# Performance work log

Hardware: AMD Instinct MI355X
Metric: run time of the kernel (lower is better)

Reference implementation:

```python
import jax, jax.numpy as jnp
import numpy as np


def adder2d(x, w, stride=1, padding=0):
    """AdderNet conv: out = -sum_{ci,kh,kw} |x_patch - w|, supports groups.
    x: [B,Cin,H,W], w: [Cout, Cin//G, K, K]. Loops only over K*K kernel taps."""
    B, Cin, H, W = x.shape
    Cout, Cin_g, K, _ = w.shape
    G = Cin // Cin_g
    Co_g = Cout // G
    xp = jnp.pad(x, ((0, 0), (0, 0), (padding, padding), (padding, padding)))
    Ho = (H + 2 * padding - K) // stride + 1
    Wo = (W + 2 * padding - K) // stride + 1
    wg = w.reshape(G, Co_g, Cin_g, K, K)
    out = jnp.zeros((B, Cout, Ho, Wo), x.dtype)
    for kh in range(K):
        for kw in range(K):
            xs = jax.lax.slice(
                xp, (0, 0, kh, kw),
                (B, Cin, kh + stride * (Ho - 1) + 1, kw + stride * (Wo - 1) + 1),
                (1, 1, stride, stride))  # [B,Cin,Ho,Wo]
            xs = xs.reshape(B, G, 1, Cin_g, Ho, Wo)
            wt = wg[:, :, :, kh, kw][None, :, :, :, None, None]  # [1,G,Co_g,Cin_g,1,1]
            out = out - jnp.abs(xs - wt).sum(3).reshape(B, Cout, Ho, Wo)
    return out


def bn(x, g, b, m, v, eps=1e-5):
    inv = g / jnp.sqrt(v + eps)
    return x * inv[None, :, None, None] + (b - m * inv)[None, :, None, None]


def setup_inputs() -> dict:
    key = jax.random.key(0)
    ks = jax.random.split(key, 18)
    d = {}
    d["x"] = jax.random.normal(ks[0], (8, 256, 28, 28), jnp.float32)
    d["w1"] = jax.random.normal(ks[1], (64, 256, 1, 1), jnp.float32) * 0.05
    d["w_peg"] = jax.random.normal(ks[2], (64, 1, 3, 3), jnp.float32) * 0.05
    d["w2"] = jax.random.normal(ks[3], (64, 64, 3, 3), jnp.float32) * 0.05
    d["w3"] = jax.random.normal(ks[4], (256, 64, 1, 1), jnp.float32) * 0.05
    for i, (c, tag) in enumerate([(64, "1"), (64, "2"), (256, "3")]):
        d["g" + tag] = jax.random.uniform(ks[5 + 4 * i], (c,), jnp.float32, 0.5, 1.5)
        d["b" + tag] = jax.random.normal(ks[6 + 4 * i], (c,), jnp.float32) * 0.1
        d["m" + tag] = jax.random.normal(ks[7 + 4 * i], (c,), jnp.float32) * 0.1
        d["v" + tag] = jax.random.uniform(ks[8 + 4 * i], (c,), jnp.float32, 0.5, 1.5)
    return d


def reference(x, w1, w_peg, w2, w3, g1, b1, m1, v1, g2, b2, m2, v2, g3, b3, m3, v3):
    residual = x  # downsample is Identity (stride=1, inplanes==outplanes)
    h = adder2d(x, w1)                       # 1x1 adder conv 256->64
    h = adder2d(h, w_peg, stride=1, padding=1)  # PEG: depthwise 3x3 adder conv
    h = jax.nn.relu(bn(h, g1, b1, m1, v1))
    h = adder2d(h, w2, padding=1)            # 3x3 adder conv 64->64
    h = jax.nn.relu(bn(h, g2, b2, m2, v2))
    h = adder2d(h, w3)                       # 1x1 adder conv 64->256
    h = bn(h, g3, b3, m3, v3)
    return jax.nn.relu(h + residual)
```

## Files before the change

### kernel.cpp

```cpp
#include <hip/hip_runtime.h>
#include <math.h>

#define PR 30
#define PC 32

__device__ __forceinline__ void tap3(const float4 a, const float2 b,
                                     const float w0, const float w1, const float w2,
                                     float4& acc) {
    acc.x += fabsf(a.x - w0) + fabsf(a.y - w1) + fabsf(a.z - w2);
    acc.y += fabsf(a.y - w0) + fabsf(a.z - w1) + fabsf(a.w - w2);
    acc.z += fabsf(a.z - w0) + fabsf(a.w - w1) + fabsf(b.x - w2);
    acc.w += fabsf(a.w - w0) + fabsf(b.x - w1) + fabsf(b.y - w2);
}

__global__ __launch_bounds__(448) void ka_fused(const float* __restrict__ x,
                                                const float* __restrict__ w1,
                                                const float* __restrict__ wpeg,
                                                const float* __restrict__ w2,
                                                const float* __restrict__ w3,
                                                const float* __restrict__ g1,
                                                const float* __restrict__ b1,
                                                const float* __restrict__ m1,
                                                const float* __restrict__ v1,
                                                float* __restrict__ h2p,
                                                float* __restrict__ w2t,
                                                float* __restrict__ w3t) {
    __shared__ __align__(16) float smem[3072];
    float* wsA = smem;
    float* h1t = smem + 1024;
    const int tid    = threadIdx.x;
    const int cobase = blockIdx.x * 4;
    const int yh     = blockIdx.y;
    const int n      = blockIdx.z;
    const int co     = tid / 112;
    const int rem    = tid % 112;
    const int row    = rem / 7;
    const int q      = rem % 7;

    {
        const int bid3 = blockIdx.x + 16 * (blockIdx.y + 2 * blockIdx.z);
        const int tg = bid3 * 448 + tid;
        if (tg < 36864) {
            int r = tg >> 6, c2 = tg & 63;
            w2t[tg] = w2[(size_t)c2 * 576 + r];
        } else if (tg < 53248) {
            int i = tg - 36864;
            int ci = i >> 8, c2 = i & 255;
            w3t[i] = w3[(size_t)c2 * 64 + ci];
        }
    }

    for (int idx = tid; idx < 1024; idx += 448) {
        int c2 = idx >> 8, ci = idx & 255;
        wsA[ci * 4 + c2] = w1[(size_t)(cobase + c2) * 256 + ci];
    }
    for (int idx = tid; idx < 512; idx += 448)
        ((float4*)h1t)[idx] = make_float4(0.f, 0.f, 0.f, 0.f);
    __syncthreads();

    const int gy = yh * 14 - 1 + row;
    if (gy >= 0 && gy < 28) {
        float4 acc = {0.f, 0.f, 0.f, 0.f};
        const float* xp = x + (size_t)n * 256 * 784 + gy * 28 + q * 4;
        #pragma unroll 8
        for (int ci = 0; ci < 256; ++ci) {
            float4 u = *(const float4*)(xp + (size_t)ci * 784);
            float w  = wsA[ci * 4 + co];
            acc.x += fabsf(u.x - w); acc.y += fabsf(u.y - w);
            acc.z += fabsf(u.z - w); acc.w += fabsf(u.w - w);
        }
        float* hd = h1t + co * 512 + row * 32 + 1 + q * 4;
        hd[0] = -acc.x; hd[1] = -acc.y; hd[2] = -acc.z; hd[3] = -acc.w;
    }
    __syncthreads();

    if (row < 14) {
        const int c  = cobase + co;
        const int oy = yh * 14 + row;
        const float* wc = wpeg + c * 9;
        const float* hb = h1t + co * 512 + row * 32 + q * 4;
        float4 acc = {0.f, 0.f, 0.f, 0.f};
        #pragma unroll
        for (int kh = 0; kh < 3; ++kh) {
            float4 a  = *(const float4*)(hb + kh * 32);
            float2 bv = *(const float2*)(hb + kh * 32 + 4);
            tap3(a, bv, wc[kh * 3 + 0], wc[kh * 3 + 1], wc[kh * 3 + 2], acc);
        }
        float inv = g1[c] * rsqrtf(v1[c] + 1e-5f);
        float bb  = b1[c] - m1[c] * inv;
        float* op = h2p + ((size_t)(n * 64 + c) * PR + oy + 1) * PC + 1 + q * 4;
        op[0] = fmaxf(-acc.x * inv + bb, 0.f);
        op[1] = fmaxf(-acc.y * inv + bb, 0.f);
        op[2] = fmaxf(-acc.z * inv + bb, 0.f);
        op[3] = fmaxf(-acc.w * inv + bb, 0.f);
    }
    for (int idx = tid; idx < 352; idx += 448) {
        if (idx < 224) {
            int rr = idx >> 4, k = idx & 15;
            int cc = k >> 2, kk = k & 3;
            int col = kk ? 28 + kk : 0;
            h2p[((size_t)(n * 64 + cobase + cc) * PR + yh * 14 + 1 + rr) * PC + col] = 0.f;
        } else {
            int j = idx - 224;
            int cc = j >> 5, col = j & 31;
            int prow = yh ? 29 : 0;
            h2p[((size_t)(n * 64 + cobase + cc) * PR + prow) * PC + col] = 0.f;
        }
    }
}

__device__ __forceinline__ void red4(float4& v, int mask) {
    v.x += __shfl_xor(v.x, mask, 64);
    v.y += __shfl_xor(v.y, mask, 64);
    v.z += __shfl_xor(v.z, mask, 64);
    v.w += __shfl_xor(v.w, mask, 64);
}

__global__ __launch_bounds__(512) void kb_fused(const float* __restrict__ h2p,
                                                const float* __restrict__ w2t,
                                                const float* __restrict__ w3t,
                                                const float* __restrict__ x,
                                                const float* __restrict__ g2,
                                                const float* __restrict__ b2,
                                                const float* __restrict__ m2,
                                                const float* __restrict__ v2,
                                                const float* __restrict__ g3,
                                                const float* __restrict__ b3,
                                                const float* __restrict__ m3,
                                                const float* __restrict__ v3,
                                                float* __restrict__ out) {
    __shared__ __align__(16) float h2t[6400];
    __shared__ __align__(16) float h3t[1280];
    const int tid  = threadIdx.x;
    const int half = blockIdx.x;
    const int Y    = blockIdx.y;
    const int n    = blockIdx.z;
    const int cic    = tid & 7;
    const int q      = (tid >> 3) & 3;
    const int colane = tid >> 5;
    const int pxb    = half * 12;

    for (int iq = tid; iq < 1536; iq += 512) {
        int ci = iq / 24, r2 = iq % 24;
        int r = r2 >> 3, c4 = r2 & 7;
        *(float4*)(h2t + ci * 100 + r * 32 + c4 * 4) =
            *(const float4*)(h2p + ((size_t)(n * 64 + ci) * PR + Y + r) * PC + c4 * 4);
    }
    __syncthreads();

    float4 acc0 = {0,0,0,0}, acc1 = acc0, acc2 = acc0, acc3 = acc0;
    #pragma unroll 2
    for (int ci8 = 0; ci8 < 8; ++ci8) {
        const int ci = ci8 * 8 + cic;
        const float* hb = h2t + ci * 100 + pxb + q * 4;
        const float* wr = w2t + (size_t)ci * 576 + colane * 4;
        #pragma unroll
        for (int kh = 0; kh < 3; ++kh) {
            float4 a  = *(const float4*)(hb + kh * 32);
            float2 bv = *(const float2*)(hb + kh * 32 + 4);
            float4 W0 = *(const float4*)(wr + (kh * 3 + 0) * 64);
            float4 W1 = *(const float4*)(wr + (kh * 3 + 1) * 64);
            float4 W2 = *(const float4*)(wr + (kh * 3 + 2) * 64);
            tap3(a, bv, W0.x, W1.x, W2.x, acc0);
            tap3(a, bv, W0.y, W1.y, W2.y, acc1);
            tap3(a, bv, W0.z, W1.z, W2.z, acc2);
            tap3(a, bv, W0.w, W1.w, W2.w, acc3);
        }
    }
    red4(acc0, 1); red4(acc0, 2); red4(acc0, 4);
    red4(acc1, 1); red4(acc1, 2); red4(acc1, 4);
    red4(acc2, 1); red4(acc2, 2); red4(acc2, 4);
    red4(acc3, 1); red4(acc3, 2); red4(acc3, 4);
    if (cic < 4) {
        float4 s = (cic == 0) ? acc0 : (cic == 1) ? acc1 : (cic == 2) ? acc2 : acc3;
        const int co = colane * 4 + cic;
        float inv = g2[co] * rsqrtf(v2[co] + 1e-5f);
        float bb  = b2[co] - m2[co] * inv;
        float4 o;
        o.x = fmaxf(-s.x * inv + bb, 0.f);
        o.y = fmaxf(-s.y * inv + bb, 0.f);
        o.z = fmaxf(-s.z * inv + bb, 0.f);
        o.w = fmaxf(-s.w * inv + bb, 0.f);
        *(float4*)(h3t + co * 20 + q * 4) = o;
    }
    __syncthreads();

    {
        const int bl  = tid >> 3;
        const int cih = (tid >> 2) & 1;
        const int bq  = tid & 3;
        float4 a0 = {0,0,0,0}, a1 = a0, a2 = a0, a3 = a0;
        const float* hb = h3t + cih * 32 * 20 + bq * 4;
        const float* wb = w3t + (size_t)(cih * 32) * 256 + bl * 4;
        #pragma unroll 8
        for (int ci_l = 0; ci_l < 32; ++ci_l) {
            float4 h = *(const float4*)(hb + ci_l * 20);
            float4 w = *(const float4*)(wb + ci_l * 256);
            a0.x += fabsf(h.x - w.x); a0.y += fabsf(h.y - w.x); a0.z += fabsf(h.z - w.x); a0.w += fabsf(h.w - w.x);
            a1.x += fabsf(h.x - w.y); a1.y += fabsf(h.y - w.y); a1.z += fabsf(h.z - w.y); a1.w += fabsf(h.w - w.y);
            a2.x += fabsf(h.x - w.z); a2.y += fabsf(h.y - w.z); a2.z += fabsf(h.z - w.z); a2.w += fabsf(h.w - w.z);
            a3.x += fabsf(h.x - w.w); a3.y += fabsf(h.y - w.w); a3.z += fabsf(h.z - w.w); a3.w += fabsf(h.w - w.w);
        }
        red4(a0, 4); red4(a1, 4); red4(a2, 4); red4(a3, 4);
        if (cih == 0) {
            float4 accs0 = a0, accs1 = a1, accs2 = a2, accs3 = a3;
            #pragma unroll
            for (int j = 0; j < 4; ++j) {
                float4 s = (j == 0) ? accs0 : (j == 1) ? accs1 : (j == 2) ? accs2 : accs3;
                const int co = bl * 4 + j;
                float inv = g3[co] * rsqrtf(v3[co] + 1e-5f);
                float bb  = b3[co] - m3[co] * inv;
                size_t obase = ((size_t)n * 256 + co) * 784 + Y * 28 + pxb + bq * 4;
                float4 r = *(const float4*)(x + obase);
                float4 o;
                o.x = fmaxf(-s.x * inv + bb + r.x, 0.f);
                o.y = fmaxf(-s.y * inv + bb + r.y, 0.f);
                o.z = fmaxf(-s.z * inv + bb + r.z, 0.f);
                o.w = fmaxf(-s.w * inv + bb + r.w, 0.f);
                *(float4*)(out + obase) = o;
            }
        }
    }
}

extern "C" void kernel_launch(void* const* d_in, const int* in_sizes, int n_in,
                              void* d_out, int out_size, void* d_ws, size_t ws_size,
                              hipStream_t stream) {
    const float* x  = (const float*)d_in[0];
    const float* w1 = (const float*)d_in[1];
    const float* wp = (const float*)d_in[2];
    const float* w2 = (const float*)d_in[3];
    const float* w3 = (const float*)d_in[4];
    const float* g1 = (const float*)d_in[5];
    const float* b1 = (const float*)d_in[6];
    const float* m1 = (const float*)d_in[7];
    const float* v1 = (const float*)d_in[8];
    const float* g2 = (const float*)d_in[9];
    const float* b2 = (const float*)d_in[10];
    const float* m2 = (const float*)d_in[11];
    const float* v2 = (const float*)d_in[12];
    const float* g3 = (const float*)d_in[13];
    const float* b3 = (const float*)d_in[14];
    const float* m3 = (const float*)d_in[15];
    const float* v3 = (const float*)d_in[16];
    float* out = (float*)d_out;

    float* wsf = (float*)d_ws;
    float* h2p = wsf;
    float* w2t = wsf + 491520;
    float* w3t = wsf + 528384;

    ka_fused<<<dim3(16, 2, 8), 448, 0, stream>>>(x, w1, wp, w2, w3,
                                                 g1, b1, m1, v1, h2p, w2t, w3t);
    kb_fused<<<dim3(2, 28, 8), 512, 0, stream>>>(h2p, w2t, w3t, x,
                                                 g2, b2, m2, v2, g3, b3, m3, v3, out);
}
```

Baseline: 71.15 us.

## Split fused 3x3+1x1 stage into separate conv and 1x1 kernels

The old kb_fused kernel did the 3x3 adder conv and the 1x1 adder conv with residual in one kernel per output row. It is replaced by two kernels: k3_conv tiles 8 output channels by 2 rows with the weights staged in shared memory, and k6 computes the 1x1 conv plus BN, residual and ReLU from an h3 intermediate held in global memory. This is meant to improve parallelism and reuse of weights in shared memory. In exchange it adds a kernel launch and a global round trip for h3, and w3 is no longer pre-transposed.

```diff
diff --git a/kernel.cpp b/kernel.cpp
--- a/kernel.cpp
+++ b/kernel.cpp
@@ -17,14 +17,12 @@
                                                 const float* __restrict__ w1,
                                                 const float* __restrict__ wpeg,
                                                 const float* __restrict__ w2,
-                                                const float* __restrict__ w3,
                                                 const float* __restrict__ g1,
                                                 const float* __restrict__ b1,
                                                 const float* __restrict__ m1,
                                                 const float* __restrict__ v1,
                                                 float* __restrict__ h2p,
-                                                float* __restrict__ w2t,
-                                                float* __restrict__ w3t) {
+                                                float* __restrict__ w2t) {
     __shared__ __align__(16) float smem[3072];
     float* wsA = smem;
     float* h1t = smem + 1024;
@@ -43,10 +41,6 @@
         if (tg < 36864) {
             int r = tg >> 6, c2 = tg & 63;
             w2t[tg] = w2[(size_t)c2 * 576 + r];
-        } else if (tg < 53248) {
-            int i = tg - 36864;
-            int ci = i >> 8, c2 = i & 255;
-            w3t[i] = w3[(size_t)c2 * 64 + ci];
         }
     }
 
@@ -109,117 +103,150 @@
     }
 }
 
-__device__ __forceinline__ void red4(float4& v, int mask) {
-    v.x += __shfl_xor(v.x, mask, 64);
-    v.y += __shfl_xor(v.y, mask, 64);
-    v.z += __shfl_xor(v.z, mask, 64);
-    v.w += __shfl_xor(v.w, mask, 64);
-}
-
-__global__ __launch_bounds__(512) void kb_fused(const float* __restrict__ h2p,
-                                                const float* __restrict__ w2t,
-                                                const float* __restrict__ w3t,
-                                                const float* __restrict__ x,
-                                                const float* __restrict__ g2,
-                                                const float* __restrict__ b2,
-                                                const float* __restrict__ m2,
-                                                const float* __restrict__ v2,
-                                                const float* __restrict__ g3,
-                                                const float* __restrict__ b3,
-                                                const float* __restrict__ m3,
-                                                const float* __restrict__ v3,
-                                                float* __restrict__ out) {
-    __shared__ __align__(16) float h2t[6400];
-    __shared__ __align__(16) float h3t[1280];
+__global__ __launch_bounds__(256) void k3_conv(const float* __restrict__ h2p,
+                                               const float* __restrict__ w2t,
+                                               const float* __restrict__ g2,
+                                               const float* __restrict__ b2,
+                                               const float* __restrict__ m2,
+                                               const float* __restrict__ v2,
+                                               float* __restrict__ h3) {
+    __shared__ __align__(16) float wt[4608];
+    __shared__ __align__(16) float h2t[8200];
+    __shared__ __align__(16) float pl[512];
     const int tid  = threadIdx.x;
-    const int half = blockIdx.x;
-    const int Y    = blockIdx.y;
-    const int n    = blockIdx.z;
-    const int cic    = tid & 7;
-    const int q      = (tid >> 3) & 3;
-    const int colane = tid >> 5;
-    const int pxb    = half * 12;
-
-    for (int iq = tid; iq < 1536; iq += 512) {
-        int ci = iq / 24, r2 = iq % 24;
-        int r = r2 >> 3, c4 = r2 & 7;
-        *(float4*)(h2t + ci * 100 + r * 32 + c4 * 4) =
-            *(const float4*)(h2p + ((size_t)(n * 64 + ci) * PR + Y + r) * PC + c4 * 4);
+    const int lane = tid & 63;
+    const int wv   = tid >> 6;
+    const int cq   = wv & 1;
+    const int cic  = wv >> 1;
+    const int col  = lane & 31;
+    const int rowl = lane >> 5;
+    const int cobase = blockIdx.x * 8;
+    const int Y0     = blockIdx.y * 2;
+    const int n      = blockIdx.z;
+    const int Y      = Y0 + rowl;
+
+    #pragma unroll
+    for (int i = 0; i < 8; ++i) {
+        int idx = i * 256 + tid;
+        int ci = idx >> 5, r2 = idx & 31, r = r2 >> 3, c4 = r2 & 7;
+        *(float4*)(h2t + ci * 128 + r * 32 + c4 * 4) =
+            *(const float4*)(h2p + ((size_t)(n * 64 + ci) * PR + Y0 + r) * PC + c4 * 4);
+    }
+    #pragma unroll
+    for (int i = 0; i < 5; ++i) {
+        int idx = i * 256 + tid;
+        if (idx < 1152) {
+            int tap = idx >> 1, c8 = (idx & 1) * 4;
+            *(float4*)(wt + tap * 8 + c8) =
+                *(const float4*)(w2t + (size_t)tap * 64 + cobase + c8);
+        }
+    }
+    __syncthreads();
+
+    float4 acc = {0.f, 0.f, 0.f, 0.f};
+    const float* hb = h2t + rowl * 32 + col;
+    const float* wb = wt + cq * 4;
+    #pragma unroll 4
+    for (int i = 0; i < 32; ++i) {
+        const int ci = cic * 32 + i;
+        const float* hr = hb + ci * 128;
+        const float* wr = wb + ci * 72;
+        #pragma unroll
+        for (int kh = 0; kh < 3; ++kh) {
+            float x0 = hr[kh * 32 + 0];
+            float x1 = hr[kh * 32 + 1];
+            float x2 = hr[kh * 32 + 2];
+            float4 w0  = *(const float4*)(wr + (kh * 3 + 0) * 8);
+            float4 w1v = *(const float4*)(wr + (kh * 3 + 1) * 8);
+            float4 w2v = *(const float4*)(wr + (kh * 3 + 2) * 8);
+            acc.x += fabsf(x0 - w0.x) + fabsf(x1 - w1v.x) + fabsf(x2 - w2v.x);
+            acc.y += fabsf(x0 - w0.y) + fabsf(x1 - w1v.y) + fabsf(x2 - w2v.y);
+            acc.z += fabsf(x0 - w0.z) + fabsf(x1 - w1v.z) + fabsf(x2 - w2v.z);
+            acc.w += fabsf(x0 - w0.w) + fabsf(x1 - w1v.w) + fabsf(x2 - w2v.w);
+        }
+    }
+    __syncthreads();
+    if (cic == 1) ((float4*)pl)[cq * 64 + lane] = acc;
+    __syncthreads();
+    if (cic == 0 && col < 28) {
+        float4 t = ((float4*)pl)[cq * 64 + lane];
+        acc.x += t.x; acc.y += t.y; acc.z += t.z; acc.w += t.w;
+        float s[4] = {acc.x, acc.y, acc.z, acc.w};
+        float* o = h3 + ((size_t)(n * 64 + cobase + cq * 4)) * 784 + Y * 28 + col;
+        #pragma unroll
+        for (int j = 0; j < 4; ++j) {
+            const int co = cobase + cq * 4 + j;
+            float inv = g2[co] * rsqrtf(v2[co] + 1e-5f);
+            float bb  = b2[co] - m2[co] * inv;
+            o[j * 784] = fmaxf(-s[j] * inv + bb, 0.f);
+        }
+    }
+}
+
+__global__ __launch_bounds__(448) void k6_adder1x1_bn_res_relu(const float* __restrict__ h3,
+                                                               const float* __restrict__ w3,
+                                                               const float* __restrict__ x,
+                                                               const float* __restrict__ g3,
+                                                               const float* __restrict__ b3,
+                                                               const float* __restrict__ m3,
+                                                               const float* __restrict__ v3,
+                                                               float* __restrict__ out) {
+    __shared__ __align__(16) float smem[7168];
+    float*  ws  = smem;
+    float4* pl4 = (float4*)smem;
+    const int tid    = threadIdx.x;
+    const int cog    = tid & 7;
+    const int pxg    = (tid >> 3) % 14;
+    const int cic    = tid / 112;
+    const int n      = blockIdx.x / 14;
+    const int p0     = (blockIdx.x % 14) * 56 + pxg * 4;
+    const int cobase = blockIdx.y * 32;
+
+    for (int idx = tid; idx < 2048; idx += 448) {
+        int co = idx >> 6, ci = idx & 63;
+        ws[ci * 36 + co] = w3[(size_t)(cobase + co) * 64 + ci];
     }
     __syncthreads();
 
     float4 acc0 = {0,0,0,0}, acc1 = acc0, acc2 = acc0, acc3 = acc0;
-    #pragma unroll 2
-    for (int ci8 = 0; ci8 < 8; ++ci8) {
-        const int ci = ci8 * 8 + cic;
-        const float* hb = h2t + ci * 100 + pxb + q * 4;
-        const float* wr = w2t + (size_t)ci * 576 + colane * 4;
-        #pragma unroll
-        for (int kh = 0; kh < 3; ++kh) {
-            float4 a  = *(const float4*)(hb + kh * 32);
-            float2 bv = *(const float2*)(hb + kh * 32 + 4);
-            float4 W0 = *(const float4*)(wr + (kh * 3 + 0) * 64);
-            float4 W1 = *(const float4*)(wr + (kh * 3 + 1) * 64);
-            float4 W2 = *(const float4*)(wr + (kh * 3 + 2) * 64);
-            tap3(a, bv, W0.x, W1.x, W2.x, acc0);
-            tap3(a, bv, W0.y, W1.y, W2.y, acc1);
-            tap3(a, bv, W0.z, W1.z, W2.z, acc2);
-            tap3(a, bv, W0.w, W1.w, W2.w, acc3);
-        }
-    }
-    red4(acc0, 1); red4(acc0, 2); red4(acc0, 4);
-    red4(acc1, 1); red4(acc1, 2); red4(acc1, 4);
-    red4(acc2, 1); red4(acc2, 2); red4(acc2, 4);
-    red4(acc3, 1); red4(acc3, 2); red4(acc3, 4);
-    if (cic < 4) {
-        float4 s = (cic == 0) ? acc0 : (cic == 1) ? acc1 : (cic == 2) ? acc2 : acc3;
-        const int co = colane * 4 + cic;
-        float inv = g2[co] * rsqrtf(v2[co] + 1e-5f);
-        float bb  = b2[co] - m2[co] * inv;
+    const float* hp = h3 + ((size_t)n * 64 + cic * 16) * 784 + p0;
+    const float* wp = ws + (cic * 16) * 36 + cog * 4;
+    #pragma unroll 8
+    for (int i = 0; i < 16; ++i) {
+        float4 u = *(const float4*)(hp + (size_t)i * 784);
+        float4 w = *(const float4*)(wp + i * 36);
+        acc0.x += fabsf(u.x - w.x); acc0.y += fabsf(u.y - w.x); acc0.z += fabsf(u.z - w.x); acc0.w += fabsf(u.w - w.x);
+        acc1.x += fabsf(u.x - w.y); acc1.y += fabsf(u.y - w.y); acc1.z += fabsf(u.z - w.y); acc1.w += fabsf(u.w - w.y);
+        acc2.x += fabsf(u.x - w.z); acc2.y += fabsf(u.y - w.z); acc2.z += fabsf(u.z - w.z); acc2.w += fabsf(u.w - w.z);
+        acc3.x += fabsf(u.x - w.w); acc3.y += fabsf(u.y - w.w); acc3.z += fabsf(u.z - w.w); acc3.w += fabsf(u.w - w.w);
+    }
+    __syncthreads();
+    const int pbase = pxg * 32 + cog * 4;
+    pl4[cic * 448 + pbase + 0] = acc0;
+    pl4[cic * 448 + pbase + 1] = acc1;
+    pl4[cic * 448 + pbase + 2] = acc2;
+    pl4[cic * 448 + pbase + 3] = acc3;
+    __syncthreads();
+
+    {
+        const int j = cic;
+        float4 s = pl4[pbase + j];
+        #pragma unroll
+        for (int c = 1; c < 4; ++c) {
+            float4 t = pl4[c * 448 + pbase + j];
+            s.x += t.x; s.y += t.y; s.z += t.z; s.w += t.w;
+        }
+        const int co = cobase + cog * 4 + j;
+        float inv = g3[co] * rsqrtf(v3[co] + 1e-5f);
+        float bb  = b3[co] - m3[co] * inv;
+        size_t obase = ((size_t)n * 256 + co) * 784 + p0;
+        float4 r = *(const float4*)(x + obase);
         float4 o;
-        o.x = fmaxf(-s.x * inv + bb, 0.f);
-        o.y = fmaxf(-s.y * inv + bb, 0.f);
-        o.z = fmaxf(-s.z * inv + bb, 0.f);
-        o.w = fmaxf(-s.w * inv + bb, 0.f);
-        *(float4*)(h3t + co * 20 + q * 4) = o;
-    }
-    __syncthreads();
-
-    {
-        const int bl  = tid >> 3;
-        const int cih = (tid >> 2) & 1;
-        const int bq  = tid & 3;
-        float4 a0 = {0,0,0,0}, a1 = a0, a2 = a0, a3 = a0;
-        const float* hb = h3t + cih * 32 * 20 + bq * 4;
-        const float* wb = w3t + (size_t)(cih * 32) * 256 + bl * 4;
-        #pragma unroll 8
-        for (int ci_l = 0; ci_l < 32; ++ci_l) {
-            float4 h = *(const float4*)(hb + ci_l * 20);
-            float4 w = *(const float4*)(wb + ci_l * 256);
-            a0.x += fabsf(h.x - w.x); a0.y += fabsf(h.y - w.x); a0.z += fabsf(h.z - w.x); a0.w += fabsf(h.w - w.x);
-            a1.x += fabsf(h.x - w.y); a1.y += fabsf(h.y - w.y); a1.z += fabsf(h.z - w.y); a1.w += fabsf(h.w - w.y);
-            a2.x += fabsf(h.x - w.z); a2.y += fabsf(h.y - w.z); a2.z += fabsf(h.z - w.z); a2.w += fabsf(h.w - w.z);
-            a3.x += fabsf(h.x - w.w); a3.y += fabsf(h.y - w.w); a3.z += fabsf(h.z - w.w); a3.w += fabsf(h.w - w.w);
-        }
-        red4(a0, 4); red4(a1, 4); red4(a2, 4); red4(a3, 4);
-        if (cih == 0) {
-            float4 accs0 = a0, accs1 = a1, accs2 = a2, accs3 = a3;
-            #pragma unroll
-            for (int j = 0; j < 4; ++j) {
-                float4 s = (j == 0) ? accs0 : (j == 1) ? accs1 : (j == 2) ? accs2 : accs3;
-                const int co = bl * 4 + j;
-                float inv = g3[co] * rsqrtf(v3[co] + 1e-5f);
-                float bb  = b3[co] - m3[co] * inv;
-                size_t obase = ((size_t)n * 256 + co) * 784 + Y * 28 + pxb + bq * 4;
-                float4 r = *(const float4*)(x + obase);
-                float4 o;
-                o.x = fmaxf(-s.x * inv + bb + r.x, 0.f);
-                o.y = fmaxf(-s.y * inv + bb + r.y, 0.f);
-                o.z = fmaxf(-s.z * inv + bb + r.z, 0.f);
-                o.w = fmaxf(-s.w * inv + bb + r.w, 0.f);
-                *(float4*)(out + obase) = o;
-            }
-        }
+        o.x = fmaxf(-s.x * inv + bb + r.x, 0.f);
+        o.y = fmaxf(-s.y * inv + bb + r.y, 0.f);
+        o.z = fmaxf(-s.z * inv + bb + r.z, 0.f);
+        o.w = fmaxf(-s.w * inv + bb + r.w, 0.f);
+        *(float4*)(out + obase) = o;
     }
 }
 
@@ -248,10 +275,10 @@
     float* wsf = (float*)d_ws;
     float* h2p = wsf;
     float* w2t = wsf + 491520;
-    float* w3t = wsf + 528384;
-
-    ka_fused<<<dim3(16, 2, 8), 448, 0, stream>>>(x, w1, wp, w2, w3,
-                                                 g1, b1, m1, v1, h2p, w2t, w3t);
-    kb_fused<<<dim3(2, 28, 8), 512, 0, stream>>>(h2p, w2t, w3t, x,
-                                                 g2, b2, m2, v2, g3, b3, m3, v3, out);
-}
+    float* h3  = wsf + 528384;
+
+    ka_fused<<<dim3(16, 2, 8), 448, 0, stream>>>(x, w1, wp, w2,
+                                                 g1, b1, m1, v1, h2p, w2t);
+    k3_conv<<<dim3(8, 14, 8), 256, 0, stream>>>(h2p, w2t, g2, b2, m2, v2, h3);
+    k6_adder1x1_bn_res_relu<<<dim3(112, 8), 448, 0, stream>>>(h3, w3, x, g3, b3, m3, v3, out);
+}
```

Result: faster. 65.14 us (-8.5%).

## Restructure kb_fused to one block per output row with LDS-staged w3

Applied to the files above, without the earlier changes.

The second kernel now handles a full 28-pixel output row per block instead of half a row, halving the grid. The 3x3 adder conv is remapped so each lane owns one column and eight output channels, with the input-channel split across wave halves and a single cross-half shuffle replacing the three-stage shuffle reduction. The 1x1 conv's weights are staged into padded shared memory and each thread loops over all 64 input channels without a reduction. This cuts shuffle traffic and redundant h2 tile loads, at the cost of much larger shared-memory use (about 100 KB per block), fewer blocks, and wasted lanes on columns 28-31 and pixel group 7.

```diff
diff --git a/kernel.cpp b/kernel.cpp
--- a/kernel.cpp
+++ b/kernel.cpp
@@ -109,13 +109,6 @@
     }
 }
 
-__device__ __forceinline__ void red4(float4& v, int mask) {
-    v.x += __shfl_xor(v.x, mask, 64);
-    v.y += __shfl_xor(v.y, mask, 64);
-    v.z += __shfl_xor(v.z, mask, 64);
-    v.w += __shfl_xor(v.w, mask, 64);
-}
-
 __global__ __launch_bounds__(512) void kb_fused(const float* __restrict__ h2p,
                                                 const float* __restrict__ w2t,
                                                 const float* __restrict__ w3t,
@@ -129,94 +122,103 @@
                                                 const float* __restrict__ m3,
                                                 const float* __restrict__ v3,
                                                 float* __restrict__ out) {
-    __shared__ __align__(16) float h2t[6400];
-    __shared__ __align__(16) float h3t[1280];
-    const int tid  = threadIdx.x;
-    const int half = blockIdx.x;
-    const int Y    = blockIdx.y;
-    const int n    = blockIdx.z;
-    const int cic    = tid & 7;
-    const int q      = (tid >> 3) & 3;
-    const int colane = tid >> 5;
-    const int pxb    = half * 12;
+    __shared__ __align__(16) float h2t[6160];
+    __shared__ __align__(16) float w3s[16896];
+    __shared__ __align__(16) float h3t[2048];
+    const int tid = threadIdx.x;
+    const int Y   = blockIdx.x;
+    const int n   = blockIdx.y;
 
     for (int iq = tid; iq < 1536; iq += 512) {
         int ci = iq / 24, r2 = iq % 24;
         int r = r2 >> 3, c4 = r2 & 7;
-        *(float4*)(h2t + ci * 100 + r * 32 + c4 * 4) =
+        *(float4*)(h2t + ci * 96 + r * 32 + c4 * 4) =
             *(const float4*)(h2p + ((size_t)(n * 64 + ci) * PR + Y + r) * PC + c4 * 4);
     }
-    __syncthreads();
-
-    float4 acc0 = {0,0,0,0}, acc1 = acc0, acc2 = acc0, acc3 = acc0;
-    #pragma unroll 2
-    for (int ci8 = 0; ci8 < 8; ++ci8) {
-        const int ci = ci8 * 8 + cic;
-        const float* hb = h2t + ci * 100 + pxb + q * 4;
-        const float* wr = w2t + (size_t)ci * 576 + colane * 4;
-        #pragma unroll
-        for (int kh = 0; kh < 3; ++kh) {
-            float4 a  = *(const float4*)(hb + kh * 32);
-            float2 bv = *(const float2*)(hb + kh * 32 + 4);
-            float4 W0 = *(const float4*)(wr + (kh * 3 + 0) * 64);
-            float4 W1 = *(const float4*)(wr + (kh * 3 + 1) * 64);
-            float4 W2 = *(const float4*)(wr + (kh * 3 + 2) * 64);
-            tap3(a, bv, W0.x, W1.x, W2.x, acc0);
-            tap3(a, bv, W0.y, W1.y, W2.y, acc1);
-            tap3(a, bv, W0.z, W1.z, W2.z, acc2);
-            tap3(a, bv, W0.w, W1.w, W2.w, acc3);
-        }
-    }
-    red4(acc0, 1); red4(acc0, 2); red4(acc0, 4);
-    red4(acc1, 1); red4(acc1, 2); red4(acc1, 4);
-    red4(acc2, 1); red4(acc2, 2); red4(acc2, 4);
-    red4(acc3, 1); red4(acc3, 2); red4(acc3, 4);
-    if (cic < 4) {
-        float4 s = (cic == 0) ? acc0 : (cic == 1) ? acc1 : (cic == 2) ? acc2 : acc3;
-        const int co = colane * 4 + cic;
-        float inv = g2[co] * rsqrtf(v2[co] + 1e-5f);
-        float bb  = b2[co] - m2[co] * inv;
-        float4 o;
-        o.x = fmaxf(-s.x * inv + bb, 0.f);
-        o.y = fmaxf(-s.y * inv + bb, 0.f);
-        o.z = fmaxf(-s.z * inv + bb, 0.f);
-        o.w = fmaxf(-s.w * inv + bb, 0.f);
-        *(float4*)(h3t + co * 20 + q * 4) = o;
+    for (int iq = tid; iq < 4096; iq += 512) {
+        int ci = iq >> 6, cq = iq & 63;
+        *(float4*)(w3s + ci * 264 + cq * 4) =
+            *(const float4*)(w3t + (size_t)ci * 256 + cq * 4);
     }
     __syncthreads();
 
     {
-        const int bl  = tid >> 3;
-        const int cih = (tid >> 2) & 1;
-        const int bq  = tid & 3;
-        float4 a0 = {0,0,0,0}, a1 = a0, a2 = a0, a3 = a0;
-        const float* hb = h3t + cih * 32 * 20 + bq * 4;
-        const float* wb = w3t + (size_t)(cih * 32) * 256 + bl * 4;
+        const int lane = tid & 63;
+        const int oct  = __builtin_amdgcn_readfirstlane(tid >> 6);
+        const int col  = lane & 31;
+        const int cih  = lane >> 5;
+        float a0 = 0.f, a1 = 0.f, a2 = 0.f, a3 = 0.f;
+        float a4 = 0.f, a5 = 0.f, a6 = 0.f, a7 = 0.f;
+        #pragma unroll 4
+        for (int i = 0; i < 32; ++i) {
+            const int ci = cih * 32 + i;
+            const float* hr = h2t + ci * 96 + col;
+            const float* wr = w2t + (size_t)ci * 576 + oct * 8;
+            #pragma unroll
+            for (int kh = 0; kh < 3; ++kh) {
+                float xw[3];
+                xw[0] = hr[kh * 32 + 0];
+                xw[1] = hr[kh * 32 + 1];
+                xw[2] = hr[kh * 32 + 2];
+                #pragma unroll
+                for (int kw = 0; kw < 3; ++kw) {
+                    const float xv = xw[kw];
+                    const float* wt = wr + (kh * 3 + kw) * 64;
+                    float4 wa = *(const float4*)(wt);
+                    float4 wb = *(const float4*)(wt + 4);
+                    a0 += fabsf(xv - wa.x); a1 += fabsf(xv - wa.y);
+                    a2 += fabsf(xv - wa.z); a3 += fabsf(xv - wa.w);
+                    a4 += fabsf(xv - wb.x); a5 += fabsf(xv - wb.y);
+                    a6 += fabsf(xv - wb.z); a7 += fabsf(xv - wb.w);
+                }
+            }
+        }
+        a0 += __shfl_xor(a0, 32, 64); a1 += __shfl_xor(a1, 32, 64);
+        a2 += __shfl_xor(a2, 32, 64); a3 += __shfl_xor(a3, 32, 64);
+        a4 += __shfl_xor(a4, 32, 64); a5 += __shfl_xor(a5, 32, 64);
+        a6 += __shfl_xor(a6, 32, 64); a7 += __shfl_xor(a7, 32, 64);
+        if (cih == 0 && col < 28) {
+            float s[8] = {a0, a1, a2, a3, a4, a5, a6, a7};
+            #pragma unroll
+            for (int j = 0; j < 8; ++j) {
+                const int cc = oct * 8 + j;
+                float inv = g2[cc] * rsqrtf(v2[cc] + 1e-5f);
+                float bb  = b2[cc] - m2[cc] * inv;
+                h3t[cc * 32 + col] = fmaxf(-s[j] * inv + bb, 0.f);
+            }
+        }
+    }
+    __syncthreads();
+
+    {
+        const int bl = tid & 63;
+        const int pg = tid >> 6;
+        float4 c0 = {0,0,0,0}, c1 = c0, c2 = c0, c3 = c0;
+        const float* hb = h3t + pg * 4;
+        const float* wb = w3s + bl * 4;
         #pragma unroll 8
-        for (int ci_l = 0; ci_l < 32; ++ci_l) {
-            float4 h = *(const float4*)(hb + ci_l * 20);
-            float4 w = *(const float4*)(wb + ci_l * 256);
-            a0.x += fabsf(h.x - w.x); a0.y += fabsf(h.y - w.x); a0.z += fabsf(h.z - w.x); a0.w += fabsf(h.w - w.x);
-            a1.x += fabsf(h.x - w.y); a1.y += fabsf(h.y - w.y); a1.z += fabsf(h.z - w.y); a1.w += fabsf(h.w - w.y);
-            a2.x += fabsf(h.x - w.z); a2.y += fabsf(h.y - w.z); a2.z += fabsf(h.z - w.z); a2.w += fabsf(h.w - w.z);
-            a3.x += fabsf(h.x - w.w); a3.y += fabsf(h.y - w.w); a3.z += fabsf(h.z - w.w); a3.w += fabsf(h.w - w.w);
-        }
-        red4(a0, 4); red4(a1, 4); red4(a2, 4); red4(a3, 4);
-        if (cih == 0) {
-            float4 accs0 = a0, accs1 = a1, accs2 = a2, accs3 = a3;
+        for (int ci = 0; ci < 64; ++ci) {
+            float4 h = *(const float4*)(hb + ci * 32);
+            float4 w = *(const float4*)(wb + ci * 264);
+            c0.x += fabsf(h.x - w.x); c0.y += fabsf(h.y - w.x); c0.z += fabsf(h.z - w.x); c0.w += fabsf(h.w - w.x);
+            c1.x += fabsf(h.x - w.y); c1.y += fabsf(h.y - w.y); c1.z += fabsf(h.z - w.y); c1.w += fabsf(h.w - w.y);
+            c2.x += fabsf(h.x - w.z); c2.y += fabsf(h.y - w.z); c2.z += fabsf(h.z - w.z); c2.w += fabsf(h.w - w.z);
+            c3.x += fabsf(h.x - w.w); c3.y += fabsf(h.y - w.w); c3.z += fabsf(h.z - w.w); c3.w += fabsf(h.w - w.w);
+        }
+        if (pg < 7) {
+            float4 accs[4] = {c0, c1, c2, c3};
             #pragma unroll
             for (int j = 0; j < 4; ++j) {
-                float4 s = (j == 0) ? accs0 : (j == 1) ? accs1 : (j == 2) ? accs2 : accs3;
                 const int co = bl * 4 + j;
                 float inv = g3[co] * rsqrtf(v3[co] + 1e-5f);
                 float bb  = b3[co] - m3[co] * inv;
-                size_t obase = ((size_t)n * 256 + co) * 784 + Y * 28 + pxb + bq * 4;
+                size_t obase = ((size_t)n * 256 + co) * 784 + Y * 28 + pg * 4;
                 float4 r = *(const float4*)(x + obase);
                 float4 o;
-                o.x = fmaxf(-s.x * inv + bb + r.x, 0.f);
-                o.y = fmaxf(-s.y * inv + bb + r.y, 0.f);
-                o.z = fmaxf(-s.z * inv + bb + r.z, 0.f);
-                o.w = fmaxf(-s.w * inv + bb + r.w, 0.f);
+                o.x = fmaxf(-accs[j].x * inv + bb + r.x, 0.f);
+                o.y = fmaxf(-accs[j].y * inv + bb + r.y, 0.f);
+                o.z = fmaxf(-accs[j].z * inv + bb + r.z, 0.f);
+                o.w = fmaxf(-accs[j].w * inv + bb + r.w, 0.f);
                 *(float4*)(out + obase) = o;
             }
         }
@@ -252,6 +254,6 @@
 
     ka_fused<<<dim3(16, 2, 8), 448, 0, stream>>>(x, w1, wp, w2, w3,
                                                  g1, b1, m1, v1, h2p, w2t, w3t);
-    kb_fused<<<dim3(2, 28, 8), 512, 0, stream>>>(h2p, w2t, w3t, x,
-                                                 g2, b2, m2, v2, g3, b3, m3, v3, out);
-}
+    kb_fused<<<dim3(28, 8), 512, 0, stream>>>(h2p, w2t, w3t, x,
+                                              g2, b2, m2, v2, g3, b3, m3, v3, out);
+}
```

New measurement: 74.56 us. +4.8%, slower.
